# Performance work log

Hardware: AMD Instinct MI355X
Metric: run time of the kernel (lower is better)

Reference implementation:

```python
import jax, jax.numpy as jnp
import numpy as np

B, S, D, H, L, V, C = 8, 1024, 768, 12, 6, 32000, 2
HD = D // H
DF = 3072
MAX_POS = 2048
EPS = 1e-5


def layer_norm(x, scale, bias):
    m = jnp.mean(x, axis=-1, keepdims=True)
    v = jnp.mean((x - m) ** 2, axis=-1, keepdims=True)
    return (x - m) / jnp.sqrt(v + EPS) * scale + bias


def setup_inputs() -> dict:
    key = jax.random.key(0)
    ks = jax.random.split(key, 16)
    std = 0.02
    return {
        "input_ids": jax.random.randint(ks[0], (B, S), 0, V),
        "attention_mask": jax.random.randint(ks[1], (B, S), 0, 2),
        "token_emb": jax.random.normal(ks[2], (V, D), jnp.float32) * std,
        "pos_emb": jax.random.normal(ks[3], (MAX_POS, D), jnp.float32) * std,
        "qkv_w": jax.random.normal(ks[4], (L, D, 3 * D), jnp.float32) * std,
        "qkv_b": jnp.zeros((L, 3 * D), jnp.float32),
        "out_w": jax.random.normal(ks[5], (L, D, D), jnp.float32) * std,
        "out_b": jnp.zeros((L, D), jnp.float32),
        "n1_s": jnp.ones((L, D), jnp.float32),
        "n1_b": jnp.zeros((L, D), jnp.float32),
        "ff1_w": jax.random.normal(ks[6], (L, D, DF), jnp.float32) * std,
        "ff1_b": jnp.zeros((L, DF), jnp.float32),
        "ff2_w": jax.random.normal(ks[7], (L, DF, D), jnp.float32) * std,
        "ff2_b": jnp.zeros((L, D), jnp.float32),
        "n2_s": jnp.ones((L, D), jnp.float32),
        "n2_b": jnp.zeros((L, D), jnp.float32),
        "hln_s": jnp.ones((D,), jnp.float32),
        "hln_b": jnp.zeros((D,), jnp.float32),
        "cls_w": jax.random.normal(ks[8], (D, C), jnp.float32) * std,
        "cls_b": jnp.zeros((C,), jnp.float32),
    }


def reference(input_ids, attention_mask, token_emb, pos_emb, qkv_w, qkv_b,
              out_w, out_b, n1_s, n1_b, ff1_w, ff1_b, ff2_w, ff2_b,
              n2_s, n2_b, hln_s, hln_b, cls_w, cls_b):
    # embeddings: token + position, scaled by sqrt(d_model)
    x = (token_emb[input_ids] + pos_emb[:S][None, :, :]) * np.float32(np.sqrt(D))
    # extended mask: 0 at valid tokens, -10000 at padding -> (B,1,1,S)
    ext = (1.0 - attention_mask.astype(x.dtype))[:, None, None, :] * -10000.0
    scale = np.float32(1.0 / np.sqrt(HD))
    for i in range(L):
        # --- self attention (pre-norm) ---
        h = layer_norm(x, n1_s[i], n1_b[i])
        qkv = (h @ qkv_w[i] + qkv_b[i]).reshape(B, S, H, 3, HD)
        q, k, v = qkv[..., 0, :], qkv[..., 1, :], qkv[..., 2, :]  # (B,S,H,HD)
        scores = jnp.einsum('bshd,bthd->bhst', q, k) * scale
        # faithful to source: masked_fill(ext_mask == 0, -1e9)
        scores = jnp.where(ext == 0, jnp.asarray(-1e9, scores.dtype), scores)
        w = jax.nn.softmax(scores, axis=-1)
        att = jnp.einsum('bhst,bthd->bshd', w, v).reshape(B, S, D)
        x = x + (att @ out_w[i] + out_b[i])
        # --- feed forward (pre-norm) ---
        h2 = layer_norm(x, n2_s[i], n2_b[i])
        ff = jax.nn.relu(h2 @ ff1_w[i] + ff1_b[i]) @ ff2_w[i] + ff2_b[i]
        x = x + ff
    # CLS pooling head
    pooled = layer_norm(x[:, 0, :], hln_s, hln_b)
    return pooled @ cls_w + cls_b
```

## Files before the change

### kernel.cpp

```cpp
#include <hip/hip_runtime.h>
#include <hip/hip_bf16.h>

typedef unsigned short u16;
typedef __bf16 bf16x8 __attribute__((ext_vector_type(8)));
typedef float f32x4 __attribute__((ext_vector_type(4)));
typedef unsigned int u32x4 __attribute__((ext_vector_type(4)));

#define DEVI __device__ __forceinline__

typedef __attribute__((address_space(3))) void lds_void;
typedef __attribute__((address_space(1))) const void gbl_void;

DEVI void gload16(const void* gp, void* lp) {
    __builtin_amdgcn_global_load_lds((gbl_void*)gp, (lds_void*)lp, 16, 0, 0);
}

DEVI u16 f2b(float f) {
    unsigned int u = __builtin_bit_cast(unsigned int, f);
    unsigned int lsb = (u >> 16) & 1u;
    u += 0x7fffu + lsb;
    return (u16)(u >> 16);
}
DEVI float b2f(u16 b) {
    unsigned int u = ((unsigned int)b) << 16;
    return __builtin_bit_cast(float, u);
}

DEVI float fexp2(float x) {
#if __has_builtin(__builtin_amdgcn_exp2f)
    return __builtin_amdgcn_exp2f(x);
#else
    return __expf(x * 0.6931471805599453f);
#endif
}

DEVI void swz_block(int& bx, int& by, int& bz) {
    const int gx = gridDim.x, gy = gridDim.y;
    const int nwg2 = gx * gy;
    int hw = blockIdx.x + gx * blockIdx.y;
    int id = (nwg2 & 7) ? hw : ((hw & 7) * (nwg2 >> 3) + (hw >> 3));
    bx = id % gx;
    by = id / gx;
    bz = blockIdx.z;
}

DEVI float blockReduceSum(float v, float* red, int tid) {
    #pragma unroll
    for (int o = 32; o; o >>= 1) v += __shfl_xor(v, o);
    __syncthreads();
    if ((tid & 63) == 0) red[tid >> 6] = v;
    __syncthreads();
    return red[0] + red[1] + red[2] + red[3];
}

__global__ void detect_kernel(const void* tok, int* flag) {
    __shared__ int bad;
    if (threadIdx.x == 0) bad = 0;
    __syncthreads();
    const u16* p = (const u16*)tok;
    int cnt = 0;
    for (int j = 0; j < 16; ++j) {
        float v = b2f(p[2 * (threadIdx.x * 16 + j)]);
        if (!(fabsf(v) < 1.0f)) cnt++;
    }
    if (cnt) atomicAdd(&bad, 1);
    __syncthreads();
    if (threadIdx.x == 0) flag[0] = (bad == 0) ? 1 : 0;
}

__global__ void to_f32_kernel(const void* src, float* dst, int n, const int* flag) {
    int i = blockIdx.x * 256 + threadIdx.x;
    if (i >= n) return;
    if (flag[0]) dst[i] = b2f(((const u16*)src)[i]);
    else         dst[i] = ((const float*)src)[i];
}

DEVI void gemm_core_async(const u16* __restrict__ A, int lda,
                          const u16* __restrict__ Bt, int ldb,
                          int K, f32x4 (&acc)[4][4],
                          u16* As, u16* Bs)
{
    const int tid  = threadIdx.x;
    const int lane = tid & 63;
    const int wave = tid >> 6;
    const int quad = lane >> 4;
    const int l16  = lane & 15;
    const int wm   = wave >> 1;
    const int wn   = wave & 1;

    const int c0 = (wave * 2 + 0) * 64 + lane;
    const int c1 = (wave * 2 + 1) * 64 + lane;
    const int r0 = c0 >> 2, h0 = (c0 & 3) * 8;
    const int r1 = c1 >> 2, h1 = (c1 & 3) * 8;

    for (int k0 = 0; k0 < K; k0 += 32) {
        __syncthreads();
        gload16(A  + (size_t)r0 * lda + k0 + h0, As + c0 * 8);
        gload16(Bt + (size_t)r0 * ldb + k0 + h0, Bs + c0 * 8);
        gload16(A  + (size_t)r1 * lda + k0 + h1, As + c1 * 8);
        gload16(Bt + (size_t)r1 * ldb + k0 + h1, Bs + c1 * 8);
        __syncthreads();

        bf16x8 af[4], bfv[4];
        #pragma unroll
        for (int mt = 0; mt < 4; ++mt)
            af[mt] = *(const bf16x8*)(As + (wm * 64 + mt * 16 + l16) * 32 + quad * 8);
        #pragma unroll
        for (int nt = 0; nt < 4; ++nt)
            bfv[nt] = *(const bf16x8*)(Bs + (wn * 64 + nt * 16 + l16) * 32 + quad * 8);
        #pragma unroll
        for (int mt = 0; mt < 4; ++mt)
            #pragma unroll
            for (int nt = 0; nt < 4; ++nt)
                acc[mt][nt] = __builtin_amdgcn_mfma_f32_16x16x32_bf16(af[mt], bfv[nt], acc[mt][nt], 0, 0, 0);
    }
}

template<int EPI>
__global__ __launch_bounds__(256) void gemm_std(
    const u16* __restrict__ A, int lda,
    const u16* __restrict__ Bt, int ldb,
    const float* __restrict__ bias,
    u16* __restrict__ outB, int ldc, int K)
{
    __shared__ u16 As[128 * 32];
    __shared__ u16 Bs[128 * 32];
    int bx, by, bz;
    swz_block(bx, by, bz);
    const size_t bM = (size_t)by * 128;
    const size_t bN = (size_t)bx * 128;
    f32x4 acc[4][4] = {};
    gemm_core_async(A + bM * lda, lda, Bt + bN * ldb, ldb, K, acc, As, Bs);

    const int tid = threadIdx.x, lane = tid & 63, wave = tid >> 6;
    const int wm = wave >> 1, wn = wave & 1, quad = lane >> 4, l16 = lane & 15;
    #pragma unroll
    for (int mt = 0; mt < 4; ++mt)
        #pragma unroll
        for (int nt = 0; nt < 4; ++nt) {
            size_t col = bN + wn * 64 + nt * 16 + l16;
            float bcol = bias[col];
            #pragma unroll
            for (int r = 0; r < 4; ++r) {
                size_t row = bM + wm * 64 + mt * 16 + quad * 4 + r;
                float v = acc[mt][nt][r] + bcol;
                if constexpr (EPI == 1) v = fmaxf(v, 0.f);
                outB[row * ldc + col] = f2b(v);
            }
        }
}

__global__ __launch_bounds__(256) void gemm_partial(
    const u16* __restrict__ A, int lda,
    const u16* __restrict__ Bt, int ldb,
    const float* __restrict__ bias,
    float* __restrict__ part, size_t pstride, int ldc, int Ksub)
{
    __shared__ u16 As[128 * 32];
    __shared__ u16 Bs[128 * 32];
    int bx, by, bz;
    swz_block(bx, by, bz);
    const size_t bM = (size_t)by * 128;
    const size_t bN = (size_t)bx * 128;
    const int Koff = bz * Ksub;
    f32x4 acc[4][4] = {};
    gemm_core_async(A + bM * lda + Koff, lda, Bt + bN * ldb + Koff, ldb, Ksub, acc, As, Bs);

    float* __restrict__ P = part + (size_t)bz * pstride;
    const int tid = threadIdx.x, lane = tid & 63, wave = tid >> 6;
    const int wm = wave >> 1, wn = wave & 1, quad = lane >> 4, l16 = lane & 15;
    const bool addb = (bz == 0);
    #pragma unroll
    for (int mt = 0; mt < 4; ++mt)
        #pragma unroll
        for (int nt = 0; nt < 4; ++nt) {
            size_t col = bN + wn * 64 + nt * 16 + l16;
            float bcol = addb ? bias[col] : 0.f;
            #pragma unroll
            for (int r = 0; r < 4; ++r) {
                size_t row = bM + wm * 64 + mt * 16 + quad * 4 + r;
                P[row * ldc + col] = acc[mt][nt][r] + bcol;
            }
        }
}

__global__ __launch_bounds__(256, 3) void flash_attn(
    const u16* __restrict__ qkv, const u16* __restrict__ vt,
    const int* __restrict__ mask, u16* __restrict__ attout)
{
    __shared__ u16 Ks[128 * 64];
    __shared__ u16 Vs[64 * 128];
    __shared__ u16 Ps[64 * 64];
    __shared__ u16 Msb[1024];

    const int bh = blockIdx.y;
    const int b = bh / 12, h = bh % 12;
    const int q0 = blockIdx.x * 64;
    const int tid = threadIdx.x, lane = tid & 63, wave = tid >> 6;
    const int quad = lane >> 4, l16 = lane & 15;
    const int sw = l16 & 7;

    for (int i = tid; i < 1024; i += 256)
        Msb[i] = (mask[b * 1024 + i] != 0) ? f2b(-1e9f) : (u16)0;

    bf16x8 aq[2];
    #pragma unroll
    for (int s = 0; s < 2; ++s)
        aq[s] = *(const bf16x8*)(qkv + (size_t)(b * 1024 + q0 + wave * 16 + l16) * 2304
                                  + h * 192 + s * 32 + quad * 8);

    const float SC2 = 0.18033688011112042f;

    float mi[4], li[4];
    f32x4 Oacc[4] = {};
    #pragma unroll
    for (int r = 0; r < 4; ++r) { mi[r] = -3e38f; li[r] = 0.f; }

    for (int kt = 0; kt < 8; ++kt) {
        u32x4 kreg[4], vreg[4];
        #pragma unroll
        for (int i = 0; i < 4; ++i) {
            int id = i * 256 + tid, row = id >> 3, ch = id & 7;
            kreg[i] = *(const u32x4*)(qkv + (size_t)(b * 1024 + kt * 128 + row) * 2304 + h * 192 + 64 + ch * 8);
        }
        #pragma unroll
        for (int i = 0; i < 4; ++i) {
            int id = i * 256 + tid, row = id >> 4, ch = id & 15;
            vreg[i] = *(const u32x4*)(vt + (size_t)bh * 65536 + (size_t)row * 1024 + kt * 128 + ch * 8);
        }
        __syncthreads();
        #pragma unroll
        for (int i = 0; i < 4; ++i) {
            int id = i * 256 + tid, row = id >> 3, ch = id & 7;
            *(u32x4*)(Ks + row * 64 + ((ch ^ (row & 7)) * 8)) = kreg[i];
        }
        #pragma unroll
        for (int i = 0; i < 4; ++i) {
            int id = i * 256 + tid, row = id >> 4, ch = id & 15;
            *(u32x4*)(Vs + row * 128 + ((ch ^ (row & 7)) * 8)) = vreg[i];
        }
        __syncthreads();

        f32x4 Sacc[8] = {};
        #pragma unroll
        for (int s = 0; s < 2; ++s) {
            bf16x8 kf[8];
            #pragma unroll
            for (int nt = 0; nt < 8; ++nt)
                kf[nt] = *(const bf16x8*)(Ks + (nt * 16 + l16) * 64 + (((s * 4 + quad) ^ sw) * 8));
            #pragma unroll
            for (int nt = 0; nt < 8; ++nt)
                Sacc[nt] = __builtin_amdgcn_mfma_f32_16x16x32_bf16(aq[s], kf[nt], Sacc[nt], 0, 0, 0);
        }

        float bias[8];
        #pragma unroll
        for (int nt = 0; nt < 8; ++nt) bias[nt] = b2f(Msb[kt * 128 + nt * 16 + l16]);
        #pragma unroll
        for (int nt = 0; nt < 8; ++nt)
            #pragma unroll
            for (int r = 0; r < 4; ++r)
                Sacc[nt][r] = fmaf(Sacc[nt][r], SC2, bias[nt]);

        float al[4];
        #pragma unroll
        for (int r = 0; r < 4; ++r) {
            float rm = fmaxf(
                fmaxf(fmaxf(Sacc[0][r], Sacc[1][r]), fmaxf(Sacc[2][r], Sacc[3][r])),
                fmaxf(fmaxf(Sacc[4][r], Sacc[5][r]), fmaxf(Sacc[6][r], Sacc[7][r])));
            #pragma unroll
            for (int o = 8; o; o >>= 1) rm = fmaxf(rm, __shfl_xor(rm, o));
            float mn = fmaxf(mi[r], rm);
            al[r] = fexp2(mi[r] - mn);
            mi[r] = mn;
            float rs = 0.f;
            #pragma unroll
            for (int nt = 0; nt < 8; ++nt) {
                float pv = fexp2(Sacc[nt][r] - mn);
                rs += pv;
                Sacc[nt][r] = pv;
            }
            #pragma unroll
            for (int o = 8; o; o >>= 1) rs += __shfl_xor(rs, o);
            li[r] = li[r] * al[r] + rs;
        }
        #pragma unroll
        for (int ntv = 0; ntv < 4; ++ntv)
            #pragma unroll
            for (int r = 0; r < 4; ++r) Oacc[ntv][r] *= al[r];

        #pragma unroll
        for (int hf = 0; hf < 2; ++hf) {
            const int rowb = wave * 16 + quad * 4;
            #pragma unroll
            for (int n4 = 0; n4 < 4; ++n4) {
                const int slot = n4 * 2 + (l16 >> 3);
                #pragma unroll
                for (int r = 0; r < 4; ++r) {
                    const int row = rowb + r;
                    Ps[row * 64 + ((slot ^ (row & 7)) * 8) + sw] = f2b(Sacc[hf * 4 + n4][r]);
                }
            }
            #pragma unroll
            for (int s2h = 0; s2h < 2; ++s2h) {
                const int s2 = hf * 2 + s2h;
                bf16x8 vf[4];
                #pragma unroll
                for (int ntv = 0; ntv < 4; ++ntv)
                    vf[ntv] = *(const bf16x8*)(Vs + (ntv * 16 + l16) * 128 + (((s2 * 4 + quad) ^ sw) * 8));
                bf16x8 pf = *(const bf16x8*)(Ps + (wave * 16 + l16) * 64 + (((s2h * 4 + quad) ^ sw) * 8));
                #pragma unroll
                for (int ntv = 0; ntv < 4; ++ntv)
                    Oacc[ntv] = __builtin_amdgcn_mfma_f32_16x16x32_bf16(pf, vf[ntv], Oacc[ntv], 0, 0, 0);
            }
        }
    }

    #pragma unroll
    for (int r = 0; r < 4; ++r) {
        float inv = 1.0f / li[r];
        int s = q0 + wave * 16 + quad * 4 + r;
        #pragma unroll
        for (int ntv = 0; ntv < 4; ++ntv)
            attout[((size_t)(b * 1024 + s)) * 768 + h * 64 + ntv * 16 + l16] = f2b(Oacc[ntv][r] * inv);
    }
}

__global__ __launch_bounds__(256) void embed_kernel(
    const int* __restrict__ ids, const void* __restrict__ tok,
    const void* __restrict__ pos, float* __restrict__ x, const int* __restrict__ flag)
{
    const int e  = blockIdx.x * 256 + threadIdx.x;
    const int bs = e / 192;
    const int d  = (e - bs * 192) * 4;
    const int s  = bs & 1023;
    const int id = ids[bs];
    float t[4], p4[4];
    if (flag[0]) {
        const u16* tb = (const u16*)tok + (size_t)id * 768 + d;
        const u16* pb = (const u16*)pos + (size_t)s  * 768 + d;
        #pragma unroll
        for (int j = 0; j < 4; ++j) { t[j] = b2f(tb[j]); p4[j] = b2f(pb[j]); }
    } else {
        const float* tb = (const float*)tok + (size_t)id * 768 + d;
        const float* pb = (const float*)pos + (size_t)s  * 768 + d;
        #pragma unroll
        for (int j = 0; j < 4; ++j) { t[j] = tb[j]; p4[j] = pb[j]; }
    }
    float* xo = x + (size_t)bs * 768 + d;
    #pragma unroll
    for (int j = 0; j < 4; ++j) xo[j] = (t[j] + p4[j]) * 27.7128129211020f;
}

__global__ __launch_bounds__(256) void layernorm_kernel(
    float* __restrict__ x, const float* __restrict__ part,
    const float* __restrict__ sc, const float* __restrict__ bi,
    u16* __restrict__ out)
{
    __shared__ float red[4];
    const size_t row = blockIdx.x;
    float* xr = x + row * 768;
    const int tid = threadIdx.x;
    float v0 = xr[tid], v1 = xr[tid + 256], v2 = xr[tid + 512];
    if (part) {
        const float* p0 = part + row * 768;
        const float* p1 = p0 + 6291456;
        v0 += p0[tid]       + p1[tid];
        v1 += p0[tid + 256] + p1[tid + 256];
        v2 += p0[tid + 512] + p1[tid + 512];
        xr[tid] = v0; xr[tid + 256] = v1; xr[tid + 512] = v2;
    }
    float s = blockReduceSum(v0 + v1 + v2, red, tid);
    float mean = s * (1.0f / 768.0f);
    float d0 = v0 - mean, d1 = v1 - mean, d2 = v2 - mean;
    float q = blockReduceSum(d0 * d0 + d1 * d1 + d2 * d2, red, tid);
    float rstd = rsqrtf(q * (1.0f / 768.0f) + 1e-5f);
    u16* orow = out + row * 768;
    orow[tid]       = f2b(d0 * rstd * sc[tid]       + bi[tid]);
    orow[tid + 256] = f2b(d1 * rstd * sc[tid + 256] + bi[tid + 256]);
    orow[tid + 512] = f2b(d2 * rstd * sc[tid + 512] + bi[tid + 512]);
}

__global__ __launch_bounds__(256) void transpose_w_kernel(
    const void* __restrict__ W, size_t off, u16* __restrict__ Wt,
    int Kd, int Nd, const int* __restrict__ flag)
{
    __shared__ u16 tile[32][34];
    const int n0 = blockIdx.x * 32, k0 = blockIdx.y * 32;
    const int tx = threadIdx.x & 31, ty = threadIdx.x >> 5;
    const int fl = flag[0];
    #pragma unroll
    for (int i = 0; i < 4; ++i) {
        size_t idx = off + (size_t)(k0 + ty + i * 8) * Nd + n0 + tx;
        u16 val = fl ? ((const u16*)W)[idx] : f2b(((const float*)W)[idx]);
        tile[ty + i * 8][tx] = val;
    }
    __syncthreads();
    #pragma unroll
    for (int i = 0; i < 4; ++i)
        Wt[(size_t)(n0 + ty + i * 8) * Kd + k0 + tx] = tile[tx][ty + i * 8];
}

__global__ __launch_bounds__(256) void build_vt_kernel(
    const u16* __restrict__ qkv, u16* __restrict__ vt)
{
    __shared__ u16 tile[64][72];
    const int bh = blockIdx.y;
    const int b = bh / 12, h = bh % 12;
    const int t0 = blockIdx.x * 64;
    const int tid = threadIdx.x;
    const int tl = tid >> 2;
    const int d4 = (tid & 3) * 16;
    const u16* src = qkv + (size_t)(b * 1024 + t0 + tl) * 2304 + h * 192 + 128 + d4;
    *(u32x4*)(&tile[tl][d4])     = *(const u32x4*)(src);
    *(u32x4*)(&tile[tl][d4 + 8]) = *(const u32x4*)(src + 8);
    __syncthreads();
    const int dd = tid >> 2;
    const int tstart = (tid & 3) * 16;
    union { u16 us[16]; u32x4 v[2]; } pk;
    #pragma unroll
    for (int j = 0; j < 16; ++j) pk.us[j] = tile[tstart + j][dd];
    u16* dst = vt + ((size_t)bh * 64 + dd) * 1024 + t0 + tstart;
    *(u32x4*)(dst)     = pk.v[0];
    *(u32x4*)(dst + 8) = pk.v[1];
}

__global__ __launch_bounds__(256) void pooled_cls_kernel(
    const float* __restrict__ x, const float* __restrict__ part,
    const float* __restrict__ hs, const float* __restrict__ hb,
    const float* __restrict__ cw, const float* __restrict__ cb, void* __restrict__ dout,
    const int* __restrict__ flag)
{
    __shared__ float red[4];
    __shared__ float pooled[768];
    const int b = blockIdx.x;
    const float* xr = x + (size_t)b * 1024 * 768;
    const float* p0 = part + (size_t)b * 1024 * 768;
    const float* p1 = p0 + 6291456;
    const int tid = threadIdx.x;
    float v0 = xr[tid]       + p0[tid]       + p1[tid];
    float v1 = xr[tid + 256] + p0[tid + 256] + p1[tid + 256];
    float v2 = xr[tid + 512] + p0[tid + 512] + p1[tid + 512];
    float s = blockReduceSum(v0 + v1 + v2, red, tid);
    float mean = s * (1.0f / 768.0f);
    float d0 = v0 - mean, d1 = v1 - mean, d2 = v2 - mean;
    float q = blockReduceSum(d0 * d0 + d1 * d1 + d2 * d2, red, tid);
    float rstd = rsqrtf(q * (1.0f / 768.0f) + 1e-5f);
    pooled[tid]       = d0 * rstd * hs[tid]       + hb[tid];
    pooled[tid + 256] = d1 * rstd * hs[tid + 256] + hb[tid + 256];
    pooled[tid + 512] = d2 * rstd * hs[tid + 512] + hb[tid + 512];
    __syncthreads();
    float q0 = 0.f, q1 = 0.f;
    for (int c = tid; c < 768; c += 256) {
        float pv = pooled[c];
        q0 += pv * cw[2 * c];
        q1 += pv * cw[2 * c + 1];
    }
    q0 = blockReduceSum(q0, red, tid);
    q1 = blockReduceSum(q1, red, tid);
    if (tid == 0) {
        float o0 = q0 + cb[0], o1 = q1 + cb[1];
        if (flag[0]) {
            ((u16*)dout)[b * 2 + 0] = f2b(o0);
            ((u16*)dout)[b * 2 + 1] = f2b(o1);
        } else {
            ((float*)dout)[b * 2 + 0] = o0;
            ((float*)dout)[b * 2 + 1] = o1;
        }
    }
}

extern "C" void kernel_launch(void* const* d_in, const int* in_sizes, int n_in,
                              void* d_out, int out_size, void* d_ws, size_t ws_size,
                              hipStream_t stream)
{
    const int* ids  = (const int*)d_in[0];
    const int* mask = (const int*)d_in[1];
    const void* tok   = d_in[2];
    const void* pos   = d_in[3];
    const void* qkv_w = d_in[4];
    const void* qkv_b = d_in[5];
    const void* out_w = d_in[6];
    const void* out_b = d_in[7];
    const void* n1_s  = d_in[8];
    const void* n1_b  = d_in[9];
    const void* ff1_w = d_in[10];
    const void* ff1_b = d_in[11];
    const void* ff2_w = d_in[12];
    const void* ff2_b = d_in[13];
    const void* n2_s  = d_in[14];
    const void* n2_b  = d_in[15];
    const void* hln_s = d_in[16];
    const void* hln_b = d_in[17];
    const void* cls_w = d_in[18];
    const void* cls_b = d_in[19];

    char* p = (char*)d_ws;
    auto alloc = [&](size_t bytes) -> char* {
        char* r = p; p += (bytes + 255) & ~(size_t)255; return r;
    };
    float* x      = (float*)alloc(6291456ull * 4);
    u16*   h      = (u16*)  alloc(6291456ull * 2);
    u16*   qkvB   = (u16*)  alloc(18874368ull * 2);
    u16*   vt     = (u16*)  alloc(6291456ull * 2);
    u16*   ffmid  = (u16*)  alloc(25165824ull * 2);
    u16*   wqkvT  = (u16*)  alloc(1769472ull * 2);
    u16*   woutT  = (u16*)  alloc(589824ull * 2);
    u16*   wff1T  = (u16*)  alloc(2359296ull * 2);
    u16*   wff2T  = (u16*)  alloc(2359296ull * 2);
    float* params = (float*)alloc(62978ull * 4);
    int*   flag   = (int*)  alloc(256);
    u16*   attout = h;

    float* Apart = (float*)ffmid;
    float* Fpart = (float*)qkvB;

    float* P_qkv_b = params + 0;
    float* P_out_b = params + 13824;
    float* P_n1_s  = params + 18432;
    float* P_n1_b  = params + 23040;
    float* P_ff1_b = params + 27648;
    float* P_ff2_b = params + 46080;
    float* P_n2_s  = params + 50688;
    float* P_n2_b  = params + 55296;
    float* P_hln_s = params + 59904;
    float* P_hln_b = params + 60672;
    float* P_cls_w = params + 61440;
    float* P_cls_b = params + 62976;

    detect_kernel<<<1, 256, 0, stream>>>(tok, flag);

    auto cvt = [&](const void* src, float* dst, int n) {
        to_f32_kernel<<<(n + 255) / 256, 256, 0, stream>>>(src, dst, n, flag);
    };
    cvt(qkv_b, P_qkv_b, 13824);  cvt(out_b, P_out_b, 4608);
    cvt(n1_s,  P_n1_s,  4608);   cvt(n1_b,  P_n1_b,  4608);
    cvt(ff1_b, P_ff1_b, 18432);  cvt(ff2_b, P_ff2_b, 4608);
    cvt(n2_s,  P_n2_s,  4608);   cvt(n2_b,  P_n2_b,  4608);
    cvt(hln_s, P_hln_s, 768);    cvt(hln_b, P_hln_b, 768);
    cvt(cls_w, P_cls_w, 1536);   cvt(cls_b, P_cls_b, 2);

    embed_kernel<<<6144, 256, 0, stream>>>(ids, tok, pos, x, flag);

    for (int l = 0; l < 6; ++l) {
        transpose_w_kernel<<<dim3(72, 24), 256, 0, stream>>>(qkv_w, (size_t)l * 1769472, wqkvT, 768, 2304, flag);
        transpose_w_kernel<<<dim3(24, 24), 256, 0, stream>>>(out_w, (size_t)l * 589824,  woutT, 768, 768,  flag);
        transpose_w_kernel<<<dim3(96, 24), 256, 0, stream>>>(ff1_w, (size_t)l * 2359296, wff1T, 768, 3072, flag);
        transpose_w_kernel<<<dim3(24, 96), 256, 0, stream>>>(ff2_w, (size_t)l * 2359296, wff2T, 3072, 768, flag);

        layernorm_kernel<<<8192, 256, 0, stream>>>(x, (l == 0) ? nullptr : Fpart,
                                                   P_n1_s + l * 768, P_n1_b + l * 768, h);
        gemm_std<0><<<dim3(18, 64), 256, 0, stream>>>(h, 768, wqkvT, 768,
                                                      P_qkv_b + l * 2304, qkvB, 2304, 768);
        build_vt_kernel<<<dim3(16, 96), 256, 0, stream>>>(qkvB, vt);
        flash_attn<<<dim3(16, 96), 256, 0, stream>>>(qkvB, vt, mask, attout);
        gemm_partial<<<dim3(6, 64, 2), 256, 0, stream>>>(attout, 768, woutT, 768,
                                                         P_out_b + l * 768, Apart, 6291456, 768, 384);
        layernorm_kernel<<<8192, 256, 0, stream>>>(x, Apart,
                                                   P_n2_s + l * 768, P_n2_b + l * 768, h);
        gemm_std<1><<<dim3(24, 64), 256, 0, stream>>>(h, 768, wff1T, 768,
                                                      P_ff1_b + l * 3072, ffmid, 3072, 768);
        gemm_partial<<<dim3(6, 64, 2), 256, 0, stream>>>(ffmid, 3072, wff2T, 3072,
                                                         P_ff2_b + l * 768, Fpart, 6291456, 768, 1536);
    }
    pooled_cls_kernel<<<8, 256, 0, stream>>>(x, Fpart, P_hln_s, P_hln_b, P_cls_w, P_cls_b, d_out, flag);
}
```

Before: 2.161 ms.

## Double-buffer K/V tiles in flash attention with async global-to-LDS loads

Flash attention now keeps two K/V tile buffers in shared memory and loads them with global_load_lds, so the next tile is fetched while the current one is computed. The separate register staging and the extra barrier per tile go away. The row-sum shuffle reduction moves out of the inner loop and runs once at the end, which is valid because the rescale factor is uniform across the 16 lanes of a row. LDS use roughly doubles, so launch bounds drop occupancy from 3 to 2 blocks per CU. One concern is that no explicit vmcnt wait appears before the barrier, so the async loads may not be guaranteed complete when they are read.

New measurement: 2.238 ms. 3.5% more time.

```diff
diff --git a/kernel.cpp b/kernel.cpp
--- a/kernel.cpp
+++ b/kernel.cpp
@@ -184,12 +184,12 @@
         }
 }
 
-__global__ __launch_bounds__(256, 3) void flash_attn(
+__global__ __launch_bounds__(256, 2) void flash_attn(
     const u16* __restrict__ qkv, const u16* __restrict__ vt,
     const int* __restrict__ mask, u16* __restrict__ attout)
 {
-    __shared__ u16 Ks[128 * 64];
-    __shared__ u16 Vs[64 * 128];
+    __shared__ u16 Ks[2][128 * 64];
+    __shared__ u16 Vs[2][64 * 128];
     __shared__ u16 Ps[64 * 64];
     __shared__ u16 Msb[1024];
 
@@ -211,43 +211,38 @@
 
     const float SC2 = 0.18033688011112042f;
 
-    float mi[4], li[4];
+    float mi[4], ls[4];
     f32x4 Oacc[4] = {};
     #pragma unroll
-    for (int r = 0; r < 4; ++r) { mi[r] = -3e38f; li[r] = 0.f; }
-
-    for (int kt = 0; kt < 8; ++kt) {
-        u32x4 kreg[4], vreg[4];
+    for (int r = 0; r < 4; ++r) { mi[r] = -3e38f; ls[r] = 0.f; }
+
+    auto STAGE = [&](int kt, int bufi) {
+        u16* Kd = &Ks[bufi][0];
+        u16* Vd = &Vs[bufi][0];
+        const u16* kb = qkv + (size_t)(b * 1024 + kt * 128) * 2304 + h * 192 + 64;
+        const u16* vb = vt + (size_t)bh * 65536 + (size_t)kt * 128;
         #pragma unroll
         for (int i = 0; i < 4; ++i) {
-            int id = i * 256 + tid, row = id >> 3, ch = id & 7;
-            kreg[i] = *(const u32x4*)(qkv + (size_t)(b * 1024 + kt * 128 + row) * 2304 + h * 192 + 64 + ch * 8);
+            int id = i * 256 + tid;
+            int row = id >> 3, chs = (id & 7) ^ (row & 7);
+            gload16(kb + (size_t)row * 2304 + chs * 8, Kd + id * 8);
         }
         #pragma unroll
         for (int i = 0; i < 4; ++i) {
-            int id = i * 256 + tid, row = id >> 4, ch = id & 15;
-            vreg[i] = *(const u32x4*)(vt + (size_t)bh * 65536 + (size_t)row * 1024 + kt * 128 + ch * 8);
-        }
-        __syncthreads();
-        #pragma unroll
-        for (int i = 0; i < 4; ++i) {
-            int id = i * 256 + tid, row = id >> 3, ch = id & 7;
-            *(u32x4*)(Ks + row * 64 + ((ch ^ (row & 7)) * 8)) = kreg[i];
-        }
-        #pragma unroll
-        for (int i = 0; i < 4; ++i) {
-            int id = i * 256 + tid, row = id >> 4, ch = id & 15;
-            *(u32x4*)(Vs + row * 128 + ((ch ^ (row & 7)) * 8)) = vreg[i];
-        }
-        __syncthreads();
-
+            int id = i * 256 + tid;
+            int row = id >> 4, chs = (id & 15) ^ (row & 7);
+            gload16(vb + (size_t)row * 1024 + chs * 8, Vd + id * 8);
+        }
+    };
+
+    auto COMPUTE = [&](int kt, const u16* Kb, const u16* Vb) {
         f32x4 Sacc[8] = {};
         #pragma unroll
         for (int s = 0; s < 2; ++s) {
             bf16x8 kf[8];
             #pragma unroll
             for (int nt = 0; nt < 8; ++nt)
-                kf[nt] = *(const bf16x8*)(Ks + (nt * 16 + l16) * 64 + (((s * 4 + quad) ^ sw) * 8));
+                kf[nt] = *(const bf16x8*)(Kb + (nt * 16 + l16) * 64 + (((s * 4 + quad) ^ sw) * 8));
             #pragma unroll
             for (int nt = 0; nt < 8; ++nt)
                 Sacc[nt] = __builtin_amdgcn_mfma_f32_16x16x32_bf16(aq[s], kf[nt], Sacc[nt], 0, 0, 0);
@@ -280,9 +275,7 @@
                 rs += pv;
                 Sacc[nt][r] = pv;
             }
-            #pragma unroll
-            for (int o = 8; o; o >>= 1) rs += __shfl_xor(rs, o);
-            li[r] = li[r] * al[r] + rs;
+            ls[r] = ls[r] * al[r] + rs;
         }
         #pragma unroll
         for (int ntv = 0; ntv < 4; ++ntv)
@@ -307,18 +300,32 @@
                 bf16x8 vf[4];
                 #pragma unroll
                 for (int ntv = 0; ntv < 4; ++ntv)
-                    vf[ntv] = *(const bf16x8*)(Vs + (ntv * 16 + l16) * 128 + (((s2 * 4 + quad) ^ sw) * 8));
+                    vf[ntv] = *(const bf16x8*)(Vb + (ntv * 16 + l16) * 128 + (((s2 * 4 + quad) ^ sw) * 8));
                 bf16x8 pf = *(const bf16x8*)(Ps + (wave * 16 + l16) * 64 + (((s2h * 4 + quad) ^ sw) * 8));
                 #pragma unroll
                 for (int ntv = 0; ntv < 4; ++ntv)
                     Oacc[ntv] = __builtin_amdgcn_mfma_f32_16x16x32_bf16(pf, vf[ntv], Oacc[ntv], 0, 0, 0);
             }
         }
+    };
+
+    STAGE(0, 0);
+    #pragma unroll 1
+    for (int kt2 = 0; kt2 < 8; kt2 += 2) {
+        __syncthreads();
+        STAGE(kt2 + 1, 1);
+        COMPUTE(kt2, &Ks[0][0], &Vs[0][0]);
+        __syncthreads();
+        if (kt2 + 2 < 8) STAGE(kt2 + 2, 0);
+        COMPUTE(kt2 + 1, &Ks[1][0], &Vs[1][0]);
     }
 
     #pragma unroll
     for (int r = 0; r < 4; ++r) {
-        float inv = 1.0f / li[r];
+        float li = ls[r];
+        #pragma unroll
+        for (int o = 8; o; o >>= 1) li += __shfl_xor(li, o);
+        float inv = 1.0f / li;
         int s = q0 + wave * 16 + quad * 4 + r;
         #pragma unroll
         for (int ntv = 0; ntv < 4; ++ntv)
```
